# Kernel tuning notes

Measured on AMD Instinct MI355X. Metric: run time of the kernel, lower is better.

Reference implementation:

```python
import jax, jax.numpy as jnp
import numpy as np

EMB = 1024
HEADS = 16
HEAD_DIM = EMB // HEADS
FF = 4 * EMB
EPS = 1e-5


def setup_inputs() -> dict:
    key = jax.random.key(0)
    ks = jax.random.split(key, 16)
    s = 0.02
    return {
        "x": jax.random.normal(ks[0], (2, 2048, EMB), dtype=jnp.float32),
        "ln1_g": jnp.ones((EMB,), jnp.float32),
        "ln1_b": jnp.zeros((EMB,), jnp.float32),
        "Wq": jax.random.normal(ks[1], (EMB, EMB), jnp.float32) * s,
        "bq": jnp.zeros((EMB,), jnp.float32),
        "Wk": jax.random.normal(ks[2], (EMB, EMB), jnp.float32) * s,
        "bk": jnp.zeros((EMB,), jnp.float32),
        "Wv": jax.random.normal(ks[3], (EMB, EMB), jnp.float32) * s,
        "bv": jnp.zeros((EMB,), jnp.float32),
        "Wo": jax.random.normal(ks[4], (EMB, EMB), jnp.float32) * s,
        "bo": jnp.zeros((EMB,), jnp.float32),
        "ln2_g": jnp.ones((EMB,), jnp.float32),
        "ln2_b": jnp.zeros((EMB,), jnp.float32),
        "W1": jax.random.normal(ks[5], (EMB, FF), jnp.float32) * s,
        "b1": jnp.zeros((FF,), jnp.float32),
        "W2": jax.random.normal(ks[6], (FF, EMB), jnp.float32) * s,
        "b2": jnp.zeros((EMB,), jnp.float32),
    }


def _layernorm(x, g, b):
    mu = jnp.mean(x, axis=-1, keepdims=True)
    var = jnp.var(x, axis=-1, keepdims=True)
    return (x - mu) * jax.lax.rsqrt(var + EPS) * g + b


def _attention(x, Wq, bq, Wk, bk, Wv, bv, Wo, bo):
    B, T, C = x.shape
    # [B,T,C] -> [B,H,T,Dh]
    def split(y):
        return y.reshape(B, T, HEADS, HEAD_DIM).transpose(0, 2, 1, 3)
    Q = split(x @ Wq + bq)
    K = split(x @ Wk + bk)
    V = split(x @ Wv + bv)
    att = jnp.einsum("bhqd,bhkd->bhqk", Q, K) / np.sqrt(HEAD_DIM).astype(np.float32)
    causal = jnp.tril(jnp.ones((T, T), bool))
    att = jnp.where(causal, att, -jnp.inf)
    att = jax.nn.softmax(att, axis=-1)
    out = jnp.einsum("bhqk,bhkd->bhqd", att, V)
    out = out.transpose(0, 2, 1, 3).reshape(B, T, C)
    return out @ Wo + bo


def reference(x, ln1_g, ln1_b, Wq, bq, Wk, bk, Wv, bv, Wo, bo,
              ln2_g, ln2_b, W1, b1, W2, b2):
    # dropout is identity in eval mode
    x = x + _attention(_layernorm(x, ln1_g, ln1_b), Wq, bq, Wk, bk, Wv, bv, Wo, bo)
    h = _layernorm(x, ln2_g, ln2_b)
    h = jax.nn.gelu(h @ W1 + b1, approximate=False) @ W2 + b2
    return x + h
```

## Files before the change

kernel.cpp:

```cpp
#include <hip/hip_runtime.h>
#include <hip/hip_bf16.h>

typedef __attribute__((ext_vector_type(4))) float f32x4;
typedef __attribute__((ext_vector_type(8))) short bf16x8;
typedef unsigned int u32;
typedef unsigned short u16;

#define GASP __attribute__((address_space(1)))
#define LASP __attribute__((address_space(3)))

__device__ __forceinline__ u16 f2bf(float f) {
  u32 u = __float_as_uint(f);
  return (u16)((u + 0x7fffu + ((u >> 16) & 1u)) >> 16);
}

__device__ __forceinline__ u32 cvtpk(float lo, float hi) {
  u32 r;
  asm("v_cvt_pk_bf16_f32 %0, %1, %2" : "=v"(r) : "v"(lo), "v"(hi));
  return r;
}

__device__ __forceinline__ void gl_lds16(const void* g, void* l) {
  __builtin_amdgcn_global_load_lds((const GASP u32*)g, (LASP u32*)l, 16, 0, 0);
}

struct CastArgs {
  const float* s[6];
  u16* d[6];
};

__global__ __launch_bounds__(256) void cast_w(CastArgs a) {
  int bid = blockIdx.x;
  int w, t, K, N, kshift;
  if (bid < 4096)      { w = bid >> 10; t = bid & 1023; K = 1024; N = 1024; kshift = 5; }
  else if (bid < 8192) { w = 4; t = bid - 4096; K = 1024; N = 4096; kshift = 5; }
  else                 { w = 5; t = bid - 8192; K = 4096; N = 1024; kshift = 7; }
  int tk = t & ((1 << kshift) - 1);
  int tn = t >> kshift;
  int k0 = tk << 5, n0 = tn << 5;
  const float* src = a.s[w];
  u16* dst = a.d[w];
  __shared__ u16 tile[32][36];
  int r = threadIdx.x >> 3, c0 = (threadIdx.x & 7) << 2;
  float4 v = *(const float4*)&src[(size_t)(k0 + r) * N + n0 + c0];
  tile[c0 + 0][r] = f2bf(v.x);
  tile[c0 + 1][r] = f2bf(v.y);
  tile[c0 + 2][r] = f2bf(v.z);
  tile[c0 + 3][r] = f2bf(v.w);
  __syncthreads();
  ushort4 o;
  o.x = tile[r][c0 + 0];
  o.y = tile[r][c0 + 1];
  o.z = tile[r][c0 + 2];
  o.w = tile[r][c0 + 3];
  *(ushort4*)&dst[(size_t)(n0 + r) * K + k0 + c0] = o;
}

__global__ __launch_bounds__(256) void ln_k(const float* __restrict__ x, const float* __restrict__ g,
                                            const float* __restrict__ b, u16* __restrict__ out) {
  int row = blockIdx.x;
  int tid = threadIdx.x;
  float4 v = *(const float4*)&x[(size_t)row * 1024 + tid * 4];
  float s = v.x + v.y + v.z + v.w;
  float ss = v.x * v.x + v.y * v.y + v.z * v.z + v.w * v.w;
#pragma unroll
  for (int o = 32; o >= 1; o >>= 1) {
    s += __shfl_xor(s, o, 64);
    ss += __shfl_xor(ss, o, 64);
  }
  __shared__ float red[8];
  int wv = tid >> 6;
  if ((tid & 63) == 0) { red[wv] = s; red[wv + 4] = ss; }
  __syncthreads();
  s = red[0] + red[1] + red[2] + red[3];
  ss = red[4] + red[5] + red[6] + red[7];
  float mu = s * (1.0f / 1024.0f);
  float var = ss * (1.0f / 1024.0f) - mu * mu;
  float rstd = rsqrtf(var + 1e-5f);
  float4 gv = *(const float4*)&g[tid * 4];
  float4 bv = *(const float4*)&b[tid * 4];
  ushort4 o4;
  o4.x = f2bf((v.x - mu) * rstd * gv.x + bv.x);
  o4.y = f2bf((v.y - mu) * rstd * gv.y + bv.y);
  o4.z = f2bf((v.z - mu) * rstd * gv.z + bv.z);
  o4.w = f2bf((v.w - mu) * rstd * gv.w + bv.w);
  *(ushort4*)&out[(size_t)row * 1024 + tid * 4] = o4;
}

template <int MODE>
__global__ __launch_bounds__(512, 2) void gemm_256(
    const u16* __restrict__ A, const u16* __restrict__ Bt,
    const float* __restrict__ bias0, const float* __restrict__ bias1, const float* __restrict__ bias2,
    void* outp, int nbx, int M, int N, int K) {
  __shared__ __align__(16) u16 As[4][256 * 32];
  __shared__ __align__(16) u16 Bs[4][256 * 32];
  const int tid = threadIdx.x;
  const int w = tid >> 6, lane = tid & 63;
  const int nwg = gridDim.x;
  const int cpx = nwg >> 3;
  const int sb = (blockIdx.x & 7) * cpx + (blockIdx.x >> 3);
  const int m0 = (sb / nbx) << 8, n0 = (sb % nbx) << 8;

  const u16* aS[2];
  const u16* bS[2];
  char* asB = (char*)As;
  char* bsB = (char*)Bs;
#pragma unroll
  for (int i = 0; i < 2; ++i) {
    int p = w * 2048 + i * 1024 + lane * 16;
    int r = p >> 6;
    int cl = ((p >> 4) & 3) ^ ((r >> 1) & 3);
    aS[i] = A + (size_t)(m0 + r) * K + cl * 8;
    bS[i] = Bt + (size_t)(n0 + r) * K + cl * 8;
  }
  f32x4 acc[8][4];
#pragma unroll
  for (int i = 0; i < 8; ++i)
#pragma unroll
    for (int j = 0; j < 4; ++j) acc[i][j] = f32x4{0.f, 0.f, 0.f, 0.f};

  const int wr = w >> 2, wc = w & 3;
  const int qi = lane & 15;
  int aOff[8], bOff[4];
#pragma unroll
  for (int mm = 0; mm < 8; ++mm) {
    int rowa = wr * 128 + mm * 16 + qi;
    aOff[mm] = rowa * 64 + (((lane >> 4) ^ ((rowa >> 1) & 3)) << 4);
  }
#pragma unroll
  for (int nn = 0; nn < 4; ++nn) {
    int rowb = wc * 64 + nn * 16 + qi;
    bOff[nn] = rowb * 64 + (((lane >> 4) ^ ((rowb >> 1) & 3)) << 4);
  }

  gl_lds16(aS[0], asB + w * 2048);
  gl_lds16(aS[1], asB + w * 2048 + 1024);
  gl_lds16(bS[0], bsB + w * 2048);
  gl_lds16(bS[1], bsB + w * 2048 + 1024);
  if (K > 32) {
    gl_lds16(aS[0] + 32, asB + 16384 + w * 2048);
    gl_lds16(aS[1] + 32, asB + 16384 + w * 2048 + 1024);
    gl_lds16(bS[0] + 32, bsB + 16384 + w * 2048);
    gl_lds16(bS[1] + 32, bsB + 16384 + w * 2048 + 1024);
  }
  if (K > 64) {
    gl_lds16(aS[0] + 64, asB + 32768 + w * 2048);
    gl_lds16(aS[1] + 64, asB + 32768 + w * 2048 + 1024);
    gl_lds16(bS[0] + 64, bsB + 32768 + w * 2048);
    gl_lds16(bS[1] + 64, bsB + 32768 + w * 2048 + 1024);
  }
  int buf = 0;
  for (int ks = 0; ks < K; ks += 32) {
    const int rem = ((K - ks) >> 5) - 1;
    if (rem >= 2)      { asm volatile("s_waitcnt vmcnt(8)" ::: "memory"); }
    else if (rem == 1) { asm volatile("s_waitcnt vmcnt(4)" ::: "memory"); }
    else               { asm volatile("s_waitcnt vmcnt(0)" ::: "memory"); }
    __builtin_amdgcn_s_barrier();
    asm volatile("" ::: "memory");
    if (ks + 96 < K) {
      const int nb = ((buf + 3) & 3) * 16384;
      gl_lds16(aS[0] + ks + 96, asB + nb + w * 2048);
      gl_lds16(aS[1] + ks + 96, asB + nb + w * 2048 + 1024);
      gl_lds16(bS[0] + ks + 96, bsB + nb + w * 2048);
      gl_lds16(bS[1] + ks + 96, bsB + nb + w * 2048 + 1024);
    }
    const int tb = buf * 16384;
    bf16x8 av[8], bv[4];
#pragma unroll
    for (int mm = 0; mm < 8; ++mm) av[mm] = *(const bf16x8*)(asB + tb + aOff[mm]);
#pragma unroll
    for (int nn = 0; nn < 4; ++nn) bv[nn] = *(const bf16x8*)(bsB + tb + bOff[nn]);
    __builtin_amdgcn_s_setprio(1);
#pragma unroll
    for (int mm = 0; mm < 8; ++mm)
#pragma unroll
      for (int nn = 0; nn < 4; ++nn)
        acc[mm][nn] = __builtin_amdgcn_mfma_f32_16x16x32_bf16(av[mm], bv[nn], acc[mm][nn], 0, 0, 0);
    __builtin_amdgcn_s_setprio(0);
    buf = (buf + 1) & 3;
  }

  const int g = lane >> 4, ci = lane & 15;
#pragma unroll
  for (int mm = 0; mm < 8; ++mm) {
#pragma unroll
    for (int nn = 0; nn < 4; ++nn) {
      int colb = n0 + wc * 64 + nn * 16 + ci;
      int rowbase = m0 + wr * 128 + mm * 16 + 4 * g;
      f32x4 c = acc[mm][nn];
      if constexpr (MODE == 2) {
        int sel = colb >> 10;
        int cc = colb & 1023;
        const float* bp = sel == 0 ? bias0 : (sel == 1 ? bias1 : bias2);
        float bb = bp[cc];
        int h = cc >> 6, d = cc & 63;
        int b_ = rowbase >> 11, tt = rowbase & 2047;
        if (sel == 2) {
          u16* op = (u16*)outp + 2ull * (4096ull * 1024ull);
          ushort4 o4;
          o4.x = f2bf(c[0] + bb);
          o4.y = f2bf(c[1] + bb);
          o4.z = f2bf(c[2] + bb);
          o4.w = f2bf(c[3] + bb);
          *(ushort4*)&op[((size_t)(b_ * 16 + h) * 64 + d) * 2048 + tt] = o4;
        } else {
          float scale = (sel == 0) ? 0.125f : 1.0f;
          u16* op = (u16*)outp + (size_t)sel * (4096ull * 1024ull);
#pragma unroll
          for (int r = 0; r < 4; ++r)
            op[((size_t)(b_ * 16 + h) * 2048 + tt + r) * 64 + d] = f2bf((c[r] + bb) * scale);
        }
      } else {
        float bb = bias0[colb];
#pragma unroll
        for (int r = 0; r < 4; ++r) {
          float v = c[r] + bb;
          float gl = 0.5f * v * (1.0f + erff(v * 0.70710678118654752f));
          ((u16*)outp)[(size_t)(rowbase + r) * N + colb] = f2bf(gl);
        }
      }
    }
  }
}

__global__ __launch_bounds__(512) void gemm_sk(
    const u16* __restrict__ A, const u16* __restrict__ Bt,
    const float* __restrict__ bias0, float* __restrict__ outp,
    const float* __restrict__ res, int M, int N, int K) {
  __shared__ __align__(16) union SM {
    struct { u16 As[2][4][128 * 32]; u16 Bs[2][4][128 * 32]; } t;
    float red[16][4][4][64];
  } sm;
  const int tid = threadIdx.x;
  const int w8 = tid >> 6, lane = tid & 63;
  const int gg = w8 >> 2, wl = w8 & 3;
  const int m0 = blockIdx.y << 7, n0 = blockIdx.x << 7;

  char* asB = (char*)sm.t.As[gg];
  char* bsB = (char*)sm.t.Bs[gg];
  const u16* aS[2];
  const u16* bS[2];
#pragma unroll
  for (int i = 0; i < 2; ++i) {
    int p = wl * 2048 + i * 1024 + lane * 16;
    int r = p >> 6;
    int cl = ((p >> 4) & 3) ^ ((r >> 1) & 3);
    aS[i] = A + (size_t)(m0 + r) * K + gg * 32 + cl * 8;
    bS[i] = Bt + (size_t)(n0 + r) * K + gg * 32 + cl * 8;
  }
  f32x4 acc[4][4];
#pragma unroll
  for (int i = 0; i < 4; ++i)
#pragma unroll
    for (int j = 0; j < 4; ++j) acc[i][j] = f32x4{0.f, 0.f, 0.f, 0.f};

  const int wr = wl >> 1, wc = wl & 1;
  int aOff[4], bOff[4];
#pragma unroll
  for (int mm = 0; mm < 4; ++mm) {
    int rowa = wr * 64 + mm * 16 + (lane & 15);
    aOff[mm] = rowa * 64 + (((lane >> 4) ^ ((rowa >> 1) & 3)) << 4);
    int rowb = wc * 64 + mm * 16 + (lane & 15);
    bOff[mm] = rowb * 64 + (((lane >> 4) ^ ((rowb >> 1) & 3)) << 4);
  }

  gl_lds16(aS[0], asB + wl * 2048);
  gl_lds16(aS[1], asB + wl * 2048 + 1024);
  gl_lds16(bS[0], bsB + wl * 2048);
  gl_lds16(bS[1], bsB + wl * 2048 + 1024);
  if (K > 64) {
    gl_lds16(aS[0] + 64, asB + 8192 + wl * 2048);
    gl_lds16(aS[1] + 64, asB + 8192 + wl * 2048 + 1024);
    gl_lds16(bS[0] + 64, bsB + 8192 + wl * 2048);
    gl_lds16(bS[1] + 64, bsB + 8192 + wl * 2048 + 1024);
  }
  if (K > 128) {
    gl_lds16(aS[0] + 128, asB + 16384 + wl * 2048);
    gl_lds16(aS[1] + 128, asB + 16384 + wl * 2048 + 1024);
    gl_lds16(bS[0] + 128, bsB + 16384 + wl * 2048);
    gl_lds16(bS[1] + 128, bsB + 16384 + wl * 2048 + 1024);
  }
  int buf = 0;
  for (int ks = 0; ks < K; ks += 64) {
    const int rem = ((K - ks) >> 6) - 1;
    if (rem >= 2)      { asm volatile("s_waitcnt vmcnt(8)" ::: "memory"); }
    else if (rem == 1) { asm volatile("s_waitcnt vmcnt(4)" ::: "memory"); }
    else               { asm volatile("s_waitcnt vmcnt(0)" ::: "memory"); }
    __builtin_amdgcn_s_barrier();
    asm volatile("" ::: "memory");
    if (ks + 192 < K) {
      const int nb = ((buf + 3) & 3) * 8192;
      gl_lds16(aS[0] + ks + 192, asB + nb + wl * 2048);
      gl_lds16(aS[1] + ks + 192, asB + nb + wl * 2048 + 1024);
      gl_lds16(bS[0] + ks + 192, bsB + nb + wl * 2048);
      gl_lds16(bS[1] + ks + 192, bsB + nb + wl * 2048 + 1024);
    }
    const int tb = buf * 8192;
    bf16x8 av[4], bv[4];
#pragma unroll
    for (int mm = 0; mm < 4; ++mm) av[mm] = *(const bf16x8*)(asB + tb + aOff[mm]);
#pragma unroll
    for (int nn = 0; nn < 4; ++nn) bv[nn] = *(const bf16x8*)(bsB + tb + bOff[nn]);
#pragma unroll
    for (int mm = 0; mm < 4; ++mm)
#pragma unroll
      for (int nn = 0; nn < 4; ++nn)
        acc[mm][nn] = __builtin_amdgcn_mfma_f32_16x16x32_bf16(av[mm], bv[nn], acc[mm][nn], 0, 0, 0);
    buf = (buf + 1) & 3;
  }

  __syncthreads();
  if (gg == 1) {
#pragma unroll
    for (int mm = 0; mm < 4; ++mm)
#pragma unroll
      for (int nn = 0; nn < 4; ++nn)
#pragma unroll
        for (int r = 0; r < 4; ++r) sm.red[mm * 4 + nn][r][wl][lane] = acc[mm][nn][r];
  }
  __syncthreads();
  if (gg == 0) {
    const int g = lane >> 4, ci = lane & 15;
#pragma unroll
    for (int mm = 0; mm < 4; ++mm) {
#pragma unroll
      for (int nn = 0; nn < 4; ++nn) {
        int colb = n0 + wc * 64 + nn * 16 + ci;
        int rowbase = m0 + wr * 64 + mm * 16 + 4 * g;
        float bb = bias0[colb];
#pragma unroll
        for (int r = 0; r < 4; ++r) {
          size_t idx = (size_t)(rowbase + r) * N + colb;
          outp[idx] = acc[mm][nn][r] + sm.red[mm * 4 + nn][r][wl][lane] + bb + res[idx];
        }
      }
    }
  }
}

__global__ __launch_bounds__(512) void attn_k(const u16* __restrict__ Q, const u16* __restrict__ Kg,
                                              const u16* __restrict__ Vt, u16* __restrict__ O) {
  __shared__ __align__(16) u16 Ks[2][64 * 64];
  __shared__ __align__(16) u16 Vs[2][64 * 64];
  const int bx = blockIdx.y;
  const int bh = blockIdx.x;
  const int tid = threadIdx.x, w = tid >> 6, lane = tid & 63;
  const int g = lane >> 4, qi = lane & 15;
  const u16* Qb = Q + (size_t)bh * 2048 * 64;
  const u16* Kb = Kg + (size_t)bh * 2048 * 64;
  const u16* Vtb = Vt + (size_t)bh * 64 * 2048;

  const int rS = tid >> 3, cS = tid & 7;
  const int csw = (cS ^ (rS & 7)) * 8;
  const u16* srcK = Kb + (size_t)rS * 64 + csw;
  const u16* srcV = Vtb + (size_t)rS * 2048 + csw;
  char* ksB = (char*)Ks;
  char* vsB = (char*)Vs;
  const int dstOff = tid * 16;

  int koff[4][2], voff[4][2];
#pragma unroll
  for (int t = 0; t < 4; ++t) {
    int row = 16 * t + qi;
#pragma unroll
    for (int h = 0; h < 2; ++h) koff[t][h] = row * 128 + (((4 * h + g) ^ (qi & 7)) << 4);
#pragma unroll
    for (int kt = 0; kt < 2; ++kt) voff[t][kt] = row * 128 + (((4 * kt + g) ^ (qi & 7)) << 4);
  }

  const int b_ = bh >> 4, hh = bh & 15;
  u32* Ou = (u32*)O;

  for (int job = 0; job < 2; ++job) {
    const int qt = job ? bx : 15 - bx;
    const int qmin = qt * 128 + w * 16;
    const int qrow = qmin + qi;
    const int qmaxw = qmin + 15;

    bf16x8 qf[2];
#pragma unroll
    for (int h = 0; h < 2; ++h)
      qf[h] = *(const bf16x8*)(Qb + (size_t)qrow * 64 + h * 32 + g * 8);

    f32x4 acc[4];
#pragma unroll
    for (int dt = 0; dt < 4; ++dt) acc[dt] = f32x4{0.f, 0.f, 0.f, 0.f};
    float m = -1e30f, lsum = 0.0f;

    __syncthreads();
    gl_lds16(srcK, ksB + dstOff);
    gl_lds16(srcV, vsB + dstOff);

    const int nsteps = 2 * qt + 2;
    int buf = 0;
    for (int s = 0; s < nsteps; ++s) {
      __syncthreads();
      if (s + 1 < nsteps) {
        int nb = buf ^ 1;
        gl_lds16(srcK + (size_t)(s + 1) * 4096, ksB + nb * 8192 + dstOff);
        gl_lds16(srcV + (size_t)(s + 1) * 64, vsB + nb * 8192 + dstOff);
      }
      const int kv0 = s * 64;
      if (kv0 <= qmaxw) {
        const int tb = buf * 8192;
        f32x4 st[4];
        __builtin_amdgcn_s_setprio(1);
#pragma unroll
        for (int t = 0; t < 4; ++t) {
          st[t] = f32x4{0.f, 0.f, 0.f, 0.f};
#pragma unroll
          for (int h = 0; h < 2; ++h) {
            bf16x8 kf = *(const bf16x8*)(ksB + tb + koff[t][h]);
            st[t] = __builtin_amdgcn_mfma_f32_16x16x32_bf16(kf, qf[h], st[t], 0, 0, 0);
          }
        }
        __builtin_amdgcn_s_setprio(0);
        float pvv[4][4];
        float tmax = -1e30f;
        if (kv0 + 63 > qmin) {
#pragma unroll
          for (int t = 0; t < 4; ++t)
#pragma unroll
            for (int r = 0; r < 4; ++r) {
              int key = kv0 + 16 * t + 4 * g + r;
              float sv = st[t][r];
              sv = (key <= qrow) ? sv : -1e30f;
              pvv[t][r] = sv;
              tmax = fmaxf(tmax, sv);
            }
        } else {
#pragma unroll
          for (int t = 0; t < 4; ++t)
#pragma unroll
            for (int r = 0; r < 4; ++r) {
              float sv = st[t][r];
              pvv[t][r] = sv;
              tmax = fmaxf(tmax, sv);
            }
        }
        tmax = fmaxf(tmax, __shfl_xor(tmax, 16, 64));
        tmax = fmaxf(tmax, __shfl_xor(tmax, 32, 64));
        if (!__all(tmax <= m + 8.0f)) {
          float mn = fmaxf(m, tmax);
          float corr = __expf(m - mn);
          lsum *= corr;
#pragma unroll
          for (int dt = 0; dt < 4; ++dt)
#pragma unroll
            for (int r = 0; r < 4; ++r) acc[dt][r] *= corr;
          m = mn;
        }
        float tsum = 0.f;
#pragma unroll
        for (int t = 0; t < 4; ++t)
#pragma unroll
          for (int r = 0; r < 4; ++r) {
            float e = __expf(pvv[t][r] - m);
            pvv[t][r] = e;
            tsum += e;
          }
        tsum += __shfl_xor(tsum, 16, 64);
        tsum += __shfl_xor(tsum, 32, 64);
        lsum += tsum;
        u32 pk[4][2], ex[4][2];
#pragma unroll
        for (int t = 0; t < 4; ++t)
#pragma unroll
          for (int p = 0; p < 2; ++p) {
            u32 v = cvtpk(pvv[t][2 * p], pvv[t][2 * p + 1]);
            pk[t][p] = v;
            ex[t][p] = (u32)__shfl_xor((int)v, 16, 64);
          }
        const bool ge = (g & 1) == 0;
        const bool G0 = (g >> 1) == 0;
        const bool innr = (g == 0) || (g == 3);
        u32 mm_[4][4];
#pragma unroll
        for (int t = 0; t < 4; ++t) {
          mm_[t][0] = ge ? pk[t][0] : ex[t][0];
          mm_[t][1] = ge ? pk[t][1] : ex[t][1];
          mm_[t][2] = ge ? ex[t][0] : pk[t][0];
          mm_[t][3] = ge ? ex[t][1] : pk[t][1];
        }
        union Frag { u32 u[4]; bf16x8 v; } f0, f1;
#pragma unroll
        for (int i = 0; i < 4; ++i) {
          u32 sel0 = G0 ? mm_[1][i] : mm_[0][i];
          u32 sel1 = G0 ? mm_[3][i] : mm_[2][i];
          u32 sw0 = (u32)__shfl_xor((int)sel0, 32, 64);
          u32 sw1 = (u32)__shfl_xor((int)sel1, 32, 64);
          u32 own0 = G0 ? mm_[0][i] : mm_[1][i];
          u32 own1 = G0 ? mm_[2][i] : mm_[3][i];
          f0.u[i] = innr ? own0 : sw0;
          f1.u[i] = innr ? own1 : sw1;
        }
        __builtin_amdgcn_s_setprio(1);
#pragma unroll
        for (int dt = 0; dt < 4; ++dt) {
          bf16x8 vfa = *(const bf16x8*)(vsB + tb + voff[dt][0]);
          acc[dt] = __builtin_amdgcn_mfma_f32_16x16x32_bf16(vfa, f0.v, acc[dt], 0, 0, 0);
          bf16x8 vfb = *(const bf16x8*)(vsB + tb + voff[dt][1]);
          acc[dt] = __builtin_amdgcn_mfma_f32_16x16x32_bf16(vfb, f1.v, acc[dt], 0, 0, 0);
        }
        __builtin_amdgcn_s_setprio(0);
      }
      buf ^= 1;
    }

    float rl = 1.0f / lsum;
    size_t rowq = (size_t)(b_ * 2048 + qrow);
#pragma unroll
    for (int dt = 0; dt < 4; ++dt) {
#pragma unroll
      for (int rp = 0; rp < 2; ++rp) {
        u16 lo = f2bf(acc[dt][rp * 2] * rl);
        u16 hi = f2bf(acc[dt][rp * 2 + 1] * rl);
        u32 pkd = (u32)lo | ((u32)hi << 16);
        size_t off = rowq * 1024 + hh * 64 + dt * 16 + 4 * g + rp * 2;
        Ou[off >> 1] = pkd;
      }
    }
  }
}

extern "C" void kernel_launch(void* const* d_in, const int* in_sizes, int n_in,
                              void* d_out, int out_size, void* d_ws, size_t ws_size,
                              hipStream_t stream) {
  const float* x    = (const float*)d_in[0];
  const float* ln1g = (const float*)d_in[1];
  const float* ln1b = (const float*)d_in[2];
  const float* Wq   = (const float*)d_in[3];
  const float* bq   = (const float*)d_in[4];
  const float* Wk   = (const float*)d_in[5];
  const float* bk   = (const float*)d_in[6];
  const float* Wv   = (const float*)d_in[7];
  const float* bv   = (const float*)d_in[8];
  const float* Wo   = (const float*)d_in[9];
  const float* bo   = (const float*)d_in[10];
  const float* ln2g = (const float*)d_in[11];
  const float* ln2b = (const float*)d_in[12];
  const float* W1   = (const float*)d_in[13];
  const float* b1   = (const float*)d_in[14];
  const float* W2   = (const float*)d_in[15];
  const float* b2   = (const float*)d_in[16];

  char* ws = (char*)d_ws;
  const size_t MB = 1ull << 20;
  u16* WqT = (u16*)(ws + 0 * MB);
  u16* WkT = (u16*)(ws + 2 * MB);
  u16* WvT = (u16*)(ws + 4 * MB);
  u16* WoT = (u16*)(ws + 6 * MB);
  u16* W1T = (u16*)(ws + 8 * MB);
  u16* W2T = (u16*)(ws + 16 * MB);
  u16* XN  = (u16*)(ws + 24 * MB);
  u16* Qb  = (u16*)(ws + 32 * MB);
  u16* Kb  = (u16*)(ws + 40 * MB);
  u16* Vtb = (u16*)(ws + 48 * MB);
  u16* Ob  = (u16*)(ws + 56 * MB);
  u16* Gb  = (u16*)(ws + 32 * MB);

  CastArgs ca;
  ca.s[0] = Wq; ca.s[1] = Wk; ca.s[2] = Wv; ca.s[3] = Wo; ca.s[4] = W1; ca.s[5] = W2;
  ca.d[0] = WqT; ca.d[1] = WkT; ca.d[2] = WvT; ca.d[3] = WoT; ca.d[4] = W1T; ca.d[5] = W2T;
  cast_w<<<12288, 256, 0, stream>>>(ca);

  ln_k<<<4096, 256, 0, stream>>>(x, ln1g, ln1b, XN);

  gemm_256<2><<<12 * 16, 512, 0, stream>>>(XN, WqT, bq, bk, bv, Qb, 12, 4096, 3072, 1024);

  attn_k<<<dim3(32, 8), 512, 0, stream>>>(Qb, Kb, Vtb, Ob);

  gemm_sk<<<dim3(8, 32), 512, 0, stream>>>(Ob, WoT, bo, (float*)d_out, x, 4096, 1024, 1024);

  ln_k<<<4096, 256, 0, stream>>>((const float*)d_out, ln2g, ln2b, XN);

  gemm_256<3><<<16 * 16, 512, 0, stream>>>(XN, W1T, b1, nullptr, nullptr, Gb, 16, 4096, 4096, 1024);

  gemm_sk<<<dim3(8, 32), 512, 0, stream>>>(Gb, W2T, b2, (float*)d_out, (const float*)d_out, 4096, 1024, 4096);
}
```

Measured before the change: 252.1 us.

## Restructure 256x256 GEMM main loop into BK=64 with staggered half-tile prefetch

The main loop of the 256x256 bf16 GEMM moves from a 4-deep ring of 32-wide K slices to 64-wide K tiles stored as 128-row halves with an 8-way XOR swizzle. Each K tile is split into four MFMA phases separated by barriers, and the next A halves and the B halves two tiles ahead are issued between phases. This spreads global-to-LDS loads across the compute and halves the number of outer iterations. The cost is more barriers per tile and a more complex wait-count scheme that must be correct for small K.

```diff
diff --git a/kernel.cpp b/kernel.cpp
--- a/kernel.cpp
+++ b/kernel.cpp
@@ -92,8 +92,10 @@
     const u16* __restrict__ A, const u16* __restrict__ Bt,
     const float* __restrict__ bias0, const float* __restrict__ bias1, const float* __restrict__ bias2,
     void* outp, int nbx, int M, int N, int K) {
-  __shared__ __align__(16) u16 As[4][256 * 32];
-  __shared__ __align__(16) u16 Bs[4][256 * 32];
+  __shared__ __align__(16) u16 As[4][128 * 64];
+  __shared__ __align__(16) u16 Bs[4][128 * 64];
+  char* asB = (char*)As;
+  char* bsB = (char*)Bs;
   const int tid = threadIdx.x;
   const int w = tid >> 6, lane = tid & 63;
   const int nwg = gridDim.x;
@@ -101,86 +103,114 @@
   const int sb = (blockIdx.x & 7) * cpx + (blockIdx.x >> 3);
   const int m0 = (sb / nbx) << 8, n0 = (sb % nbx) << 8;
 
-  const u16* aS[2];
-  const u16* bS[2];
-  char* asB = (char*)As;
-  char* bsB = (char*)Bs;
-#pragma unroll
-  for (int i = 0; i < 2; ++i) {
-    int p = w * 2048 + i * 1024 + lane * 16;
-    int r = p >> 6;
-    int cl = ((p >> 4) & 3) ^ ((r >> 1) & 3);
-    aS[i] = A + (size_t)(m0 + r) * K + cl * 8;
-    bS[i] = Bt + (size_t)(n0 + r) * K + cl * 8;
-  }
+  const int rA = tid >> 3;
+  const int csw = ((tid & 7) ^ (rA & 7)) * 8;
+  const u16* pA = A + (size_t)(m0 + rA) * K + csw;
+  const u16* pB = Bt + (size_t)(n0 + rA) * K + csw;
+  const int dstOff = tid * 16;
+
+#define STG_A(kt, h, d_) do {                                            \
+    const u16* s_ = pA + (size_t)((h) * 128) * K + (size_t)(kt) * 64;    \
+    char* l_ = asB + ((d_) * 2 + (h)) * 16384 + dstOff;                  \
+    gl_lds16(s_, l_);                                                    \
+    gl_lds16(s_ + (size_t)64 * K, l_ + 8192);                            \
+  } while (0)
+#define STG_B(kt, h, d_) do {                                            \
+    const u16* s_ = pB + (size_t)((h) * 128) * K + (size_t)(kt) * 64;    \
+    char* l_ = bsB + ((d_) * 2 + (h)) * 16384 + dstOff;                  \
+    gl_lds16(s_, l_);                                                    \
+    gl_lds16(s_ + (size_t)64 * K, l_ + 8192);                            \
+  } while (0)
+
+  const int wr = w >> 2, wc = w & 3;
+  const int g = lane >> 4, qi = lane & 15;
+
+  int aOff[8][2], bOff[4][2];
+#pragma unroll
+  for (int mm = 0; mm < 8; ++mm) {
+    int row = mm * 16 + qi;
+#pragma unroll
+    for (int ks = 0; ks < 2; ++ks)
+      aOff[mm][ks] = row * 128 + (((ks * 4 + g) ^ (qi & 7)) << 4);
+  }
+#pragma unroll
+  for (int nn = 0; nn < 4; ++nn) {
+    int rowb = (wc & 1) * 64 + nn * 16 + qi;
+#pragma unroll
+    for (int ks = 0; ks < 2; ++ks)
+      bOff[nn][ks] = rowb * 128 + (((ks * 4 + g) ^ (qi & 7)) << 4);
+  }
+
   f32x4 acc[8][4];
 #pragma unroll
   for (int i = 0; i < 8; ++i)
 #pragma unroll
     for (int j = 0; j < 4; ++j) acc[i][j] = f32x4{0.f, 0.f, 0.f, 0.f};
 
-  const int wr = w >> 2, wc = w & 3;
-  const int qi = lane & 15;
-  int aOff[8], bOff[4];
-#pragma unroll
-  for (int mm = 0; mm < 8; ++mm) {
-    int rowa = wr * 128 + mm * 16 + qi;
-    aOff[mm] = rowa * 64 + (((lane >> 4) ^ ((rowa >> 1) & 3)) << 4);
-  }
-#pragma unroll
-  for (int nn = 0; nn < 4; ++nn) {
-    int rowb = wc * 64 + nn * 16 + qi;
-    bOff[nn] = rowb * 64 + (((lane >> 4) ^ ((rowb >> 1) & 3)) << 4);
-  }
-
-  gl_lds16(aS[0], asB + w * 2048);
-  gl_lds16(aS[1], asB + w * 2048 + 1024);
-  gl_lds16(bS[0], bsB + w * 2048);
-  gl_lds16(bS[1], bsB + w * 2048 + 1024);
-  if (K > 32) {
-    gl_lds16(aS[0] + 32, asB + 16384 + w * 2048);
-    gl_lds16(aS[1] + 32, asB + 16384 + w * 2048 + 1024);
-    gl_lds16(bS[0] + 32, bsB + 16384 + w * 2048);
-    gl_lds16(bS[1] + 32, bsB + 16384 + w * 2048 + 1024);
-  }
-  if (K > 64) {
-    gl_lds16(aS[0] + 64, asB + 32768 + w * 2048);
-    gl_lds16(aS[1] + 64, asB + 32768 + w * 2048 + 1024);
-    gl_lds16(bS[0] + 64, bsB + 32768 + w * 2048);
-    gl_lds16(bS[1] + 64, bsB + 32768 + w * 2048 + 1024);
-  }
-  int buf = 0;
-  for (int ks = 0; ks < K; ks += 32) {
-    const int rem = ((K - ks) >> 5) - 1;
-    if (rem >= 2)      { asm volatile("s_waitcnt vmcnt(8)" ::: "memory"); }
-    else if (rem == 1) { asm volatile("s_waitcnt vmcnt(4)" ::: "memory"); }
-    else               { asm volatile("s_waitcnt vmcnt(0)" ::: "memory"); }
+#define PHASE(MB) do {                                                                   \
+    bf16x8 a00 = *(const bf16x8*)(asB + aTB + aOff[(MB)][0]);                            \
+    bf16x8 a01 = *(const bf16x8*)(asB + aTB + aOff[(MB)][1]);                            \
+    bf16x8 a10 = *(const bf16x8*)(asB + aTB + aOff[(MB) + 1][0]);                        \
+    bf16x8 a11 = *(const bf16x8*)(asB + aTB + aOff[(MB) + 1][1]);                        \
+    __builtin_amdgcn_s_setprio(1);                                                       \
+    acc[(MB)][0] = __builtin_amdgcn_mfma_f32_16x16x32_bf16(a00, bv[0][0], acc[(MB)][0], 0, 0, 0); \
+    acc[(MB)][1] = __builtin_amdgcn_mfma_f32_16x16x32_bf16(a00, bv[1][0], acc[(MB)][1], 0, 0, 0); \
+    acc[(MB)][2] = __builtin_amdgcn_mfma_f32_16x16x32_bf16(a00, bv[2][0], acc[(MB)][2], 0, 0, 0); \
+    acc[(MB)][3] = __builtin_amdgcn_mfma_f32_16x16x32_bf16(a00, bv[3][0], acc[(MB)][3], 0, 0, 0); \
+    acc[(MB) + 1][0] = __builtin_amdgcn_mfma_f32_16x16x32_bf16(a10, bv[0][0], acc[(MB) + 1][0], 0, 0, 0); \
+    acc[(MB) + 1][1] = __builtin_amdgcn_mfma_f32_16x16x32_bf16(a10, bv[1][0], acc[(MB) + 1][1], 0, 0, 0); \
+    acc[(MB) + 1][2] = __builtin_amdgcn_mfma_f32_16x16x32_bf16(a10, bv[2][0], acc[(MB) + 1][2], 0, 0, 0); \
+    acc[(MB) + 1][3] = __builtin_amdgcn_mfma_f32_16x16x32_bf16(a10, bv[3][0], acc[(MB) + 1][3], 0, 0, 0); \
+    acc[(MB)][0] = __builtin_amdgcn_mfma_f32_16x16x32_bf16(a01, bv[0][1], acc[(MB)][0], 0, 0, 0); \
+    acc[(MB)][1] = __builtin_amdgcn_mfma_f32_16x16x32_bf16(a01, bv[1][1], acc[(MB)][1], 0, 0, 0); \
+    acc[(MB)][2] = __builtin_amdgcn_mfma_f32_16x16x32_bf16(a01, bv[2][1], acc[(MB)][2], 0, 0, 0); \
+    acc[(MB)][3] = __builtin_amdgcn_mfma_f32_16x16x32_bf16(a01, bv[3][1], acc[(MB)][3], 0, 0, 0); \
+    acc[(MB) + 1][0] = __builtin_amdgcn_mfma_f32_16x16x32_bf16(a11, bv[0][1], acc[(MB) + 1][0], 0, 0, 0); \
+    acc[(MB) + 1][1] = __builtin_amdgcn_mfma_f32_16x16x32_bf16(a11, bv[1][1], acc[(MB) + 1][1], 0, 0, 0); \
+    acc[(MB) + 1][2] = __builtin_amdgcn_mfma_f32_16x16x32_bf16(a11, bv[2][1], acc[(MB) + 1][2], 0, 0, 0); \
+    acc[(MB) + 1][3] = __builtin_amdgcn_mfma_f32_16x16x32_bf16(a11, bv[3][1], acc[(MB) + 1][3], 0, 0, 0); \
+    __builtin_amdgcn_s_setprio(0);                                                       \
+  } while (0)
+
+  const int T = K >> 6;
+  STG_A(0, 0, 0); STG_A(0, 1, 0);
+  STG_B(0, 0, 0); STG_B(0, 1, 0);
+  if (T > 1) { STG_B(1, 0, 1); STG_B(1, 1, 1); }
+
+  for (int t = 0; t < T; ++t) {
+    const int d = t & 1;
+    const int aTB = (d * 2 + wr) * 16384;
+    const int bTB = (d * 2 + (wc >> 1)) * 16384;
+    if (t < T - 1) { asm volatile("s_waitcnt vmcnt(4)" ::: "memory"); }
+    else           { asm volatile("s_waitcnt vmcnt(0)" ::: "memory"); }
     __builtin_amdgcn_s_barrier();
     asm volatile("" ::: "memory");
-    if (ks + 96 < K) {
-      const int nb = ((buf + 3) & 3) * 16384;
-      gl_lds16(aS[0] + ks + 96, asB + nb + w * 2048);
-      gl_lds16(aS[1] + ks + 96, asB + nb + w * 2048 + 1024);
-      gl_lds16(bS[0] + ks + 96, bsB + nb + w * 2048);
-      gl_lds16(bS[1] + ks + 96, bsB + nb + w * 2048 + 1024);
+    if (t + 1 < T) STG_A(t + 1, 0, d ^ 1);
+    bf16x8 bv[4][2];
+#pragma unroll
+    for (int nn = 0; nn < 4; ++nn) {
+      bv[nn][0] = *(const bf16x8*)(bsB + bTB + bOff[nn][0]);
+      bv[nn][1] = *(const bf16x8*)(bsB + bTB + bOff[nn][1]);
     }
-    const int tb = buf * 16384;
-    bf16x8 av[8], bv[4];
-#pragma unroll
-    for (int mm = 0; mm < 8; ++mm) av[mm] = *(const bf16x8*)(asB + tb + aOff[mm]);
-#pragma unroll
-    for (int nn = 0; nn < 4; ++nn) bv[nn] = *(const bf16x8*)(bsB + tb + bOff[nn]);
-    __builtin_amdgcn_s_setprio(1);
-#pragma unroll
-    for (int mm = 0; mm < 8; ++mm)
-#pragma unroll
-      for (int nn = 0; nn < 4; ++nn)
-        acc[mm][nn] = __builtin_amdgcn_mfma_f32_16x16x32_bf16(av[mm], bv[nn], acc[mm][nn], 0, 0, 0);
-    __builtin_amdgcn_s_setprio(0);
-    buf = (buf + 1) & 3;
-  }
-
-  const int g = lane >> 4, ci = lane & 15;
+    PHASE(0);
+    __builtin_amdgcn_s_barrier();
+    asm volatile("" ::: "memory");
+    if (t + 1 < T) STG_A(t + 1, 1, d ^ 1);
+    PHASE(2);
+    __builtin_amdgcn_s_barrier();
+    asm volatile("" ::: "memory");
+    if (t + 2 < T) STG_B(t + 2, 0, d);
+    PHASE(4);
+    __builtin_amdgcn_s_barrier();
+    asm volatile("" ::: "memory");
+    if (t + 2 < T) STG_B(t + 2, 1, d);
+    PHASE(6);
+  }
+#undef PHASE
+#undef STG_A
+#undef STG_B
+
+  const int ci = lane & 15;
 #pragma unroll
   for (int mm = 0; mm < 8; ++mm) {
 #pragma unroll
@@ -193,7 +223,7 @@
         int cc = colb & 1023;
         const float* bp = sel == 0 ? bias0 : (sel == 1 ? bias1 : bias2);
         float bb = bp[cc];
-        int h = cc >> 6, d = cc & 63;
+        int h = cc >> 6, dd = cc & 63;
         int b_ = rowbase >> 11, tt = rowbase & 2047;
         if (sel == 2) {
           u16* op = (u16*)outp + 2ull * (4096ull * 1024ull);
@@ -202,13 +232,13 @@
           o4.y = f2bf(c[1] + bb);
           o4.z = f2bf(c[2] + bb);
           o4.w = f2bf(c[3] + bb);
-          *(ushort4*)&op[((size_t)(b_ * 16 + h) * 64 + d) * 2048 + tt] = o4;
+          *(ushort4*)&op[((size_t)(b_ * 16 + h) * 64 + dd) * 2048 + tt] = o4;
         } else {
           float scale = (sel == 0) ? 0.125f : 1.0f;
           u16* op = (u16*)outp + (size_t)sel * (4096ull * 1024ull);
 #pragma unroll
           for (int r = 0; r < 4; ++r)
-            op[((size_t)(b_ * 16 + h) * 2048 + tt + r) * 64 + d] = f2bf((c[r] + bb) * scale);
+            op[((size_t)(b_ * 16 + h) * 2048 + tt + r) * 64 + dd] = f2bf((c[r] + bb) * scale);
         }
       } else {
         float bb = bias0[colb];
```

Result: no change. 247.5 us (-1.8%).
